# Kernel tuning notes

Hardware: AMD Instinct MI355X
Metric: run time of the kernel (lower is better)

Reference implementation:

```python
import jax, jax.numpy as jnp
import numpy as np

NUM_HEADS = 12
NUM_LANDMARKS = 64
DIM = 768


def _iterative_inv(mat, n_iter=6):
    # mat: [B, H, L, L]
    L = mat.shape[-1]
    I = jnp.eye(L, dtype=mat.dtype)
    K = mat
    # init: V = K^T / max_j(sum_i K_ij), scalar per (B, H)
    denom = jnp.max(jnp.sum(K, axis=-2), axis=-1)[:, :, None, None]
    V = (1.0 / denom) * jnp.swapaxes(K, -1, -2)
    for _ in range(n_iter):
        KV = jnp.matmul(K, V)
        V = jnp.matmul(0.25 * V, 13.0 * I - jnp.matmul(KV, 15.0 * I - jnp.matmul(KV, 7.0 * I - KV)))
    return V


def setup_inputs() -> dict:
    key = jax.random.key(0)
    k1, k2, k3, k4 = jax.random.split(key, 4)
    B, N, C = 4, 4096, DIM
    x = jax.random.normal(k1, (B, N, C), dtype=jnp.float32)
    w_qkv = jax.random.normal(k2, (3 * C, C), dtype=jnp.float32) * (C ** -0.5)
    w_proj = jax.random.normal(k3, (C, C), dtype=jnp.float32) * (C ** -0.5)
    b_proj = jax.random.normal(k4, (C,), dtype=jnp.float32) * 0.01
    return {"x": x, "w_qkv": w_qkv, "w_proj": w_proj, "b_proj": b_proj}


def reference(x, w_qkv, w_proj, b_proj):
    B, N, C = x.shape
    H, Lm = NUM_HEADS, NUM_LANDMARKS
    hd = C // H
    scale = hd ** 0.5
    # qkv: [3, B, H, N, hd]
    qkv = (x @ w_qkv.T).reshape(B, N, 3, H, hd).transpose(2, 0, 3, 1, 4)
    q, k, v = qkv[0], qkv[1], qkv[2]
    q = q / scale  # scaling happens BEFORE landmark pooling, as in source
    segs = N // Lm  # N % Lm == 0 path
    keys_landmarks = k.reshape(B, H, Lm, segs, hd).mean(axis=-2)      # [B,H,Lm,hd]
    queries_landmarks = q.reshape(B, H, Lm, segs, hd).mean(axis=-2)   # [B,H,Lm,hd]
    kernel_1 = jax.nn.softmax(jnp.einsum('bhnd,bhld->bhnl', q, keys_landmarks), axis=-1)            # [B,H,N,Lm]
    kernel_2 = jax.nn.softmax(jnp.einsum('bhmd,bhld->bhml', queries_landmarks, keys_landmarks), axis=-1)  # [B,H,Lm,Lm]
    kernel_3 = jax.nn.softmax(jnp.einsum('bhld,bhnd->bhln', queries_landmarks, k), axis=-1)         # [B,H,Lm,N]
    out = jnp.matmul(jnp.matmul(kernel_1, _iterative_inv(kernel_2)), jnp.matmul(kernel_3, v))       # [B,H,N,hd]
    out = out.transpose(0, 2, 1, 3).reshape(B, N, C)
    return out @ w_proj.T + b_proj
```

## Files before the change

kernel.cpp:

```cpp
#include <hip/hip_runtime.h>
#include <hip/hip_bf16.h>

#define DI __device__ __forceinline__

typedef __attribute__((ext_vector_type(8))) short bh8;
typedef __attribute__((ext_vector_type(8))) unsigned short us8;
typedef __attribute__((ext_vector_type(4))) float f4ev;

static constexpr int Bn = 4;
static constexpr int Nn = 4096;
static constexpr int Cn = 768;
static constexpr int Hn = 12;
static constexpr int Dn = 64;
static constexpr int Ln = 64;
static constexpr int TOKS = Bn * Nn;
static constexpr int BHn = Bn * Hn;

static constexpr size_t SZ_XB  = (size_t)TOKS * Cn * 2;
static constexpr size_t SZ_QKV = (size_t)BHn * Nn * Dn * 2;
static constexpr size_t OFF_XB   = 0;
static constexpr size_t OFF_QB   = OFF_XB + SZ_XB;
static constexpr size_t OFF_KB   = OFF_QB + SZ_QKV;
static constexpr size_t OFF_VB   = OFF_KB + SZ_QKV;
static constexpr size_t OFF_WQB  = OFF_VB + SZ_QKV;
static constexpr size_t OFF_WPB  = OFF_WQB + (size_t)3 * Cn * Cn * 2;
static constexpr size_t OFF_XM   = OFF_WPB + (size_t)Cn * Cn * 2;
static constexpr size_t OFF_QL   = OFF_XM + (size_t)Bn * Ln * Cn * 4;
static constexpr size_t OFF_KL   = OFF_QL + (size_t)Bn * Ln * Cn * 4;
static constexpr size_t OFF_VINV = OFF_KL + (size_t)Bn * Ln * Cn * 4;
static constexpr size_t OFF_CP   = OFF_VINV + (size_t)BHn * 64 * 64 * 4;
static constexpr size_t OFF_W2   = OFF_CP + (size_t)BHn * 32 * 64 * 2 * 4;

DI unsigned short f2bf(float f) {
  __hip_bfloat16 h = __float2bfloat16(f);
  return *reinterpret_cast<unsigned short*>(&h);
}
DI float bf2f(unsigned short u) {
  union { unsigned int i; float f; } c; c.i = ((unsigned)u) << 16; return c.f;
}

DI void gload_lds16(const void* g, void* l) {
  __builtin_amdgcn_global_load_lds((const __attribute__((address_space(1))) void*)g,
                                   (__attribute__((address_space(3))) void*)l, 16, 0, 0);
}

__global__ void castw_k(const float* __restrict__ wqkv, const float* __restrict__ wproj,
                        unsigned short* __restrict__ dq, unsigned short* __restrict__ dp) {
  const int nq = 3 * Cn * Cn / 4;
  const int np = Cn * Cn / 4;
  int i = blockIdx.x * blockDim.x + threadIdx.x;
  int st = gridDim.x * blockDim.x;
  for (; i < nq + np; i += st) {
    const float4* s4;
    ushort4* d4;
    int idx;
    if (i < nq) { s4 = (const float4*)wqkv;  d4 = (ushort4*)dq; idx = i; }
    else        { s4 = (const float4*)wproj; d4 = (ushort4*)dp; idx = i - nq; }
    float4 v = s4[idx];
    ushort4 o; o.x = f2bf(v.x); o.y = f2bf(v.y); o.z = f2bf(v.z); o.w = f2bf(v.w);
    d4[idx] = o;
  }
}

__global__ void castmean_k(const float* __restrict__ x, unsigned short* __restrict__ xb,
                           float* __restrict__ xm) {
  int bl = blockIdx.x, cz = blockIdx.y;
  int c = cz * 384 + threadIdx.x * 2;
  const float* xp = x + (size_t)bl * 64 * Cn + c;
  unsigned short* xbp = xb + (size_t)bl * 64 * Cn + c;
  float s0 = 0.f, s1 = 0.f;
  #pragma unroll 8
  for (int r = 0; r < 64; ++r) {
    float2 v = *(const float2*)(xp + (size_t)r * Cn);
    ushort2 o; o.x = f2bf(v.x); o.y = f2bf(v.y);
    *(ushort2*)(xbp + (size_t)r * Cn) = o;
    s0 += v.x; s1 += v.y;
  }
  xm[(size_t)bl * Cn + c]     = s0 * 0.015625f;
  xm[(size_t)bl * Cn + c + 1] = s1 * 0.015625f;
}

__launch_bounds__(256)
__global__ void landgemm_k(const float* __restrict__ xm, const float* __restrict__ wqkv,
                           float* __restrict__ part) {
  __shared__ float XT[64][65];
  __shared__ float WT[64][65];
  int b = blockIdx.x, ct = blockIdx.y, kc = blockIdx.z;
  int t = threadIdx.x;
  int tr = t >> 4, tc = t & 15;
  int r0 = tr * 4, j0 = tc * 4;
  const float* xb_ = xm + (size_t)b * Ln * Cn + kc * 64;
  const float* wb_ = wqkv + (size_t)ct * 64 * Cn + kc * 64;
  #pragma unroll
  for (int i = t; i < 1024; i += 256) {
    int r = i >> 4, c4 = (i & 15) * 4;
    float4 xv = *(const float4*)(xb_ + (size_t)r * Cn + c4);
    XT[c4 + 0][r] = xv.x; XT[c4 + 1][r] = xv.y; XT[c4 + 2][r] = xv.z; XT[c4 + 3][r] = xv.w;
    float4 wv = *(const float4*)(wb_ + (size_t)r * Cn + c4);
    WT[c4 + 0][r] = wv.x; WT[c4 + 1][r] = wv.y; WT[c4 + 2][r] = wv.z; WT[c4 + 3][r] = wv.w;
  }
  __syncthreads();
  float acc[4][4];
  #pragma unroll
  for (int i = 0; i < 4; ++i)
    #pragma unroll
    for (int j = 0; j < 4; ++j) acc[i][j] = 0.f;
  for (int cc = 0; cc < 64; ++cc) {
    float4 a4 = *(const float4*)&XT[cc][r0];
    float4 b4 = *(const float4*)&WT[cc][j0];
    acc[0][0] += a4.x * b4.x; acc[0][1] += a4.x * b4.y; acc[0][2] += a4.x * b4.z; acc[0][3] += a4.x * b4.w;
    acc[1][0] += a4.y * b4.x; acc[1][1] += a4.y * b4.y; acc[1][2] += a4.y * b4.z; acc[1][3] += a4.y * b4.w;
    acc[2][0] += a4.z * b4.x; acc[2][1] += a4.z * b4.y; acc[2][2] += a4.z * b4.z; acc[2][3] += a4.z * b4.w;
    acc[3][0] += a4.w * b4.x; acc[3][1] += a4.w * b4.y; acc[3][2] += a4.w * b4.z; acc[3][3] += a4.w * b4.w;
  }
  float* op = part + ((size_t)kc * 256 + b * Ln) * 1536 + (size_t)ct * 64;
  #pragma unroll
  for (int i = 0; i < 4; ++i)
    *(float4*)(op + (size_t)(r0 + i) * 1536 + j0) = make_float4(acc[i][0], acc[i][1], acc[i][2], acc[i][3]);
}

__global__ void landred_k(const float* __restrict__ part, float* __restrict__ ql,
                          float* __restrict__ kl) {
  int i4 = blockIdx.x * 256 + threadIdx.x;
  const float4* p4 = (const float4*)part;
  float4 s = p4[i4];
  #pragma unroll
  for (int kc = 1; kc < 12; ++kc) {
    float4 v = p4[(size_t)kc * 98304 + i4];
    s.x += v.x; s.y += v.y; s.z += v.z; s.w += v.w;
  }
  int row = i4 / 384, c = (i4 % 384) * 4;
  if (c < 768) {
    s.x *= 0.125f; s.y *= 0.125f; s.z *= 0.125f; s.w *= 0.125f;
    *(float4*)(ql + (size_t)row * Cn + c) = s;
  } else {
    *(float4*)(kl + (size_t)row * Cn + (c - 768)) = s;
  }
}

__launch_bounds__(256)
__global__ void k2inv_k(const float* __restrict__ ql, const float* __restrict__ kl,
                        float* __restrict__ vinv) {
  __shared__ float B0[64][68], B1[64][68], B2[64][68], B3[64][68],
                   B4[64][68], B5[64][68], B6[64][68], B7[64][68];
  __shared__ float dinv_s;
  float (*Qt)[68] = B0, (*Kt)[68] = B1;
  float (*KV)[68] = B0, (*KVt)[68] = B1;
  float (*K2)[68] = B2, (*K2t)[68] = B3;
  float (*Vv)[68] = B4, (*Vt)[68] = B5;
  float (*T1)[68] = B6, (*Uu)[68] = B7;

  int bh = blockIdx.x, b = bh / Hn, h = bh % Hn;
  int t = threadIdx.x;
  int tr = t >> 4, tc = t & 15;
  int r0 = tr * 4, j0 = tc * 4;

  {
    const float* qbase = ql + (size_t)(b * Ln) * Cn + h * Dn;
    const float* kbase = kl + (size_t)(b * Ln) * Cn + h * Dn;
    #pragma unroll
    for (int it = 0; it < 4; ++it) {
      int idx = it * 256 + t;
      int l = idx >> 4, d0 = (idx & 15) * 4;
      float4 qv = *(const float4*)(qbase + (size_t)l * Cn + d0);
      float4 kv = *(const float4*)(kbase + (size_t)l * Cn + d0);
      Qt[d0 + 0][l] = qv.x; Qt[d0 + 1][l] = qv.y; Qt[d0 + 2][l] = qv.z; Qt[d0 + 3][l] = qv.w;
      Kt[d0 + 0][l] = kv.x; Kt[d0 + 1][l] = kv.y; Kt[d0 + 2][l] = kv.z; Kt[d0 + 3][l] = kv.w;
    }
  }
  __syncthreads();

  float acc[4][4];
  #define MM64(LT, RR)                                                     \
    {                                                                      \
      _Pragma("unroll")                                                    \
      for (int i_ = 0; i_ < 4; ++i_)                                       \
        _Pragma("unroll")                                                  \
        for (int j_ = 0; j_ < 4; ++j_) acc[i_][j_] = 0.f;                  \
      for (int c_ = 0; c_ < 64; c_ += 4) {                                 \
        _Pragma("unroll")                                                  \
        for (int cc_ = 0; cc_ < 4; ++cc_) {                                \
          float4 a4 = *(const float4*)&LT[c_ + cc_][r0];                   \
          float4 b4 = *(const float4*)&RR[c_ + cc_][j0];                   \
          acc[0][0] += a4.x * b4.x; acc[0][1] += a4.x * b4.y;              \
          acc[0][2] += a4.x * b4.z; acc[0][3] += a4.x * b4.w;              \
          acc[1][0] += a4.y * b4.x; acc[1][1] += a4.y * b4.y;              \
          acc[1][2] += a4.y * b4.z; acc[1][3] += a4.y * b4.w;              \
          acc[2][0] += a4.z * b4.x; acc[2][1] += a4.z * b4.y;              \
          acc[2][2] += a4.z * b4.z; acc[2][3] += a4.z * b4.w;              \
          acc[3][0] += a4.w * b4.x; acc[3][1] += a4.w * b4.y;              \
          acc[3][2] += a4.w * b4.z; acc[3][3] += a4.w * b4.w;              \
        }                                                                  \
      }                                                                    \
    }

  MM64(Qt, Kt);
  #pragma unroll
  for (int i = 0; i < 4; ++i)
    *(float4*)&K2[r0 + i][j0] = make_float4(acc[i][0], acc[i][1], acc[i][2], acc[i][3]);
  __syncthreads();

  if (t < 64) {
    float m = -1e30f;
    #pragma unroll
    for (int c4 = 0; c4 < 16; ++c4) {
      float4 v = *(const float4*)&K2[t][c4 * 4];
      m = fmaxf(m, fmaxf(fmaxf(v.x, v.y), fmaxf(v.z, v.w)));
    }
    float s = 0.f;
    #pragma unroll
    for (int c4 = 0; c4 < 16; ++c4) {
      float4 v = *(const float4*)&K2[t][c4 * 4];
      v.x = __expf(v.x - m); v.y = __expf(v.y - m);
      v.z = __expf(v.z - m); v.w = __expf(v.w - m);
      s += v.x + v.y + v.z + v.w;
      *(float4*)&K2[t][c4 * 4] = v;
    }
    float inv = 1.f / s;
    #pragma unroll
    for (int c4 = 0; c4 < 16; ++c4) {
      float4 v = *(const float4*)&K2[t][c4 * 4];
      v.x *= inv; v.y *= inv; v.z *= inv; v.w *= inv;
      *(float4*)&K2[t][c4 * 4] = v;
      K2t[c4 * 4 + 0][t] = v.x; K2t[c4 * 4 + 1][t] = v.y;
      K2t[c4 * 4 + 2][t] = v.z; K2t[c4 * 4 + 3][t] = v.w;
    }
  }
  __syncthreads();
  if (t < 64) {
    float cs = 0.f;
    #pragma unroll
    for (int c4 = 0; c4 < 16; ++c4) {
      float4 v = *(const float4*)&K2t[t][c4 * 4];
      cs += v.x + v.y + v.z + v.w;
    }
    #pragma unroll
    for (int off = 1; off < 64; off <<= 1) cs = fmaxf(cs, __shfl_xor(cs, off));
    if (t == 0) dinv_s = 1.f / cs;
  }
  __syncthreads();
  float dinv = dinv_s;
  #pragma unroll
  for (int jj = 0; jj < 4; ++jj) {
    float4 k4 = *(const float4*)&K2[j0 + jj][r0];
    k4.x *= dinv; k4.y *= dinv; k4.z *= dinv; k4.w *= dinv;
    *(float4*)&Vt[j0 + jj][r0] = k4;
    Vv[r0 + 0][j0 + jj] = k4.x; Vv[r0 + 1][j0 + jj] = k4.y;
    Vv[r0 + 2][j0 + jj] = k4.z; Vv[r0 + 3][j0 + jj] = k4.w;
  }
  __syncthreads();

  float nv[4][4];
  for (int itn = 0; itn < 6; ++itn) {
    MM64(K2t, Vv);
    #pragma unroll
    for (int i = 0; i < 4; ++i)
      *(float4*)&KV[r0 + i][j0] = make_float4(acc[i][0], acc[i][1], acc[i][2], acc[i][3]);
    #pragma unroll
    for (int jj = 0; jj < 4; ++jj)
      *(float4*)&KVt[j0 + jj][r0] = make_float4(acc[0][jj], acc[1][jj], acc[2][jj], acc[3][jj]);
    __syncthreads();
    MM64(KVt, KV);
    #pragma unroll
    for (int i = 0; i < 4; ++i) {
      float4 kv4 = *(const float4*)&KV[r0 + i][j0];
      *(float4*)&T1[r0 + i][j0] = make_float4(7.f * kv4.x - acc[i][0], 7.f * kv4.y - acc[i][1],
                                              7.f * kv4.z - acc[i][2], 7.f * kv4.w - acc[i][3]);
    }
    __syncthreads();
    MM64(KVt, T1);
    #pragma unroll
    for (int i = 0; i < 4; ++i) {
      float4 kv4 = *(const float4*)&KV[r0 + i][j0];
      *(float4*)&Uu[r0 + i][j0] = make_float4(15.f * kv4.x - acc[i][0], 15.f * kv4.y - acc[i][1],
                                              15.f * kv4.z - acc[i][2], 15.f * kv4.w - acc[i][3]);
    }
    __syncthreads();
    MM64(Vt, Uu);
    #pragma unroll
    for (int i = 0; i < 4; ++i) {
      float4 v4 = *(const float4*)&Vv[r0 + i][j0];
      nv[i][0] = 0.25f * (13.f * v4.x - acc[i][0]);
      nv[i][1] = 0.25f * (13.f * v4.y - acc[i][1]);
      nv[i][2] = 0.25f * (13.f * v4.z - acc[i][2]);
      nv[i][3] = 0.25f * (13.f * v4.w - acc[i][3]);
    }
    __syncthreads();
    #pragma unroll
    for (int i = 0; i < 4; ++i)
      *(float4*)&Vv[r0 + i][j0] = make_float4(nv[i][0], nv[i][1], nv[i][2], nv[i][3]);
    #pragma unroll
    for (int jj = 0; jj < 4; ++jj)
      *(float4*)&Vt[j0 + jj][r0] = make_float4(nv[0][jj], nv[1][jj], nv[2][jj], nv[3][jj]);
    __syncthreads();
  }
  float* op = vinv + (size_t)bh * 4096;
  #pragma unroll
  for (int i = 0; i < 4; ++i)
    *(float4*)(op + (size_t)(r0 + i) * 64 + j0) = make_float4(nv[i][0], nv[i][1], nv[i][2], nv[i][3]);
  #undef MM64
}

__launch_bounds__(256)
__global__ void gemm_qkv_k(const __hip_bfloat16* __restrict__ A, const __hip_bfloat16* __restrict__ W,
                           __hip_bfloat16* __restrict__ qb, __hip_bfloat16* __restrict__ kb,
                           __hip_bfloat16* __restrict__ vb) {
  __shared__ unsigned short As[2][128][64], Bs[2][128][64];
  int t = threadIdx.x, lane = t & 63, w = t >> 6;
  int wr = w >> 1, wc = w & 1;
  int m0 = blockIdx.x * 128, n0 = blockIdx.y * 128;
  int srow = w * 8 + (lane >> 3);
  int scol = ((lane & 7) ^ ((lane >> 3) & 7)) * 8;
  f4ev acc[4][4];
  f4ev zz = {0.f, 0.f, 0.f, 0.f};
  #pragma unroll
  for (int m = 0; m < 4; ++m)
    #pragma unroll
    for (int n = 0; n < 4; ++n) acc[m][n] = zz;
  const __hip_bfloat16* ga = A + (size_t)(m0 + srow) * Cn + scol;
  const __hip_bfloat16* gb = W + (size_t)(n0 + srow) * Cn + scol;

  #pragma unroll
  for (int c = 0; c < 4; ++c) {
    gload_lds16(ga + (size_t)(c * 32) * Cn, &As[0][c * 32 + w * 8][0]);
    gload_lds16(gb + (size_t)(c * 32) * Cn, &Bs[0][c * 32 + w * 8][0]);
  }
  asm volatile("s_waitcnt vmcnt(0)" ::: "memory");
  __builtin_amdgcn_s_barrier();
  int cur = 0;
  for (int it = 0; it < 12; ++it) {
    if (it < 11) {
      int k0 = (it + 1) * 64;
      #pragma unroll
      for (int c = 0; c < 4; ++c) {
        gload_lds16(ga + (size_t)(c * 32) * Cn + k0, &As[cur ^ 1][c * 32 + w * 8][0]);
        gload_lds16(gb + (size_t)(c * 32) * Cn + k0, &Bs[cur ^ 1][c * 32 + w * 8][0]);
      }
      asm volatile("s_waitcnt vmcnt(8)" ::: "memory");
    } else {
      asm volatile("s_waitcnt vmcnt(0)" ::: "memory");
    }
    __builtin_amdgcn_s_barrier();
    #pragma unroll
    for (int ks = 0; ks < 2; ++ks) {
      int pc = ((ks * 4 + (lane >> 4)) ^ (lane & 7)) * 8;
      bh8 af[4], bf_[4];
      #pragma unroll
      for (int m = 0; m < 4; ++m)
        af[m] = *(const bh8*)&As[cur][wr * 64 + m * 16 + (lane & 15)][pc];
      #pragma unroll
      for (int n = 0; n < 4; ++n)
        bf_[n] = *(const bh8*)&Bs[cur][wc * 64 + n * 16 + (lane & 15)][pc];
      #pragma unroll
      for (int m = 0; m < 4; ++m)
        #pragma unroll
        for (int n = 0; n < 4; ++n)
          acc[m][n] = __builtin_amdgcn_mfma_f32_16x16x32_bf16(af[m], bf_[n], acc[m][n], 0, 0, 0);
    }
    asm volatile("s_waitcnt lgkmcnt(0)" ::: "memory");
    __builtin_amdgcn_s_barrier();
    cur ^= 1;
  }
  int which = (n0 >= 1536) ? 2 : (n0 >= 768 ? 1 : 0);
  __hip_bfloat16* dst = which == 0 ? qb : (which == 1 ? kb : vb);
  float sc = which == 0 ? 0.125f : 1.f;
  #pragma unroll
  for (int m = 0; m < 4; ++m) {
    int rbase = m0 + wr * 64 + m * 16 + ((lane >> 4) << 2);
    #pragma unroll
    for (int n = 0; n < 4; ++n) {
      int c = n0 + wc * 64 + n * 16 + (lane & 15);
      int rem = c - which * 768;
      int h = rem >> 6, dd = rem & 63;
      #pragma unroll
      for (int jj = 0; jj < 4; ++jj) {
        int r = rbase + jj;
        int b = r >> 12, ntok = r & 4095;
        dst[(((size_t)(b * Hn + h) * Nn + ntok) << 6) + dd] = __float2bfloat16(acc[m][n][jj] * sc);
      }
    }
  }
}

__launch_bounds__(256)
__global__ void k3vflash_k(const float* __restrict__ ql, const __hip_bfloat16* __restrict__ kb,
                           const __hip_bfloat16* __restrict__ vb,
                           float* __restrict__ ocp, float* __restrict__ stat) {
  __shared__ unsigned short Ks[128][72];
  __shared__ unsigned short VT[64][136];
  auto Pl = (unsigned short (*)[136]) & Ks[0][0];
  int ch = blockIdx.x, bh = blockIdx.y;
  int b = bh / Hn, h = bh % Hn;
  int t = threadIdx.x, lane = t & 63, w = t >> 6;

  {
    int row = t >> 1, half = (t & 1) * 32;
    const us8* krow = (const us8*)((const unsigned short*)kb + ((size_t)bh * Nn + (size_t)ch * 128 + row) * Dn + half);
    const us8* vrow = (const us8*)((const unsigned short*)vb + ((size_t)bh * Nn + (size_t)ch * 128 + row) * Dn + half);
    us8 kv0 = krow[0], kv1 = krow[1], kv2 = krow[2], kv3 = krow[3];
    us8 vv0 = vrow[0], vv1 = vrow[1], vv2 = vrow[2], vv3 = vrow[3];
    *(us8*)&Ks[row][half + 0]  = kv0;
    *(us8*)&Ks[row][half + 8]  = kv1;
    *(us8*)&Ks[row][half + 16] = kv2;
    *(us8*)&Ks[row][half + 24] = kv3;
    #pragma unroll
    for (int e = 0; e < 8; ++e) {
      VT[half + e][row]      = vv0[e];
      VT[half + 8 + e][row]  = vv1[e];
      VT[half + 16 + e][row] = vv2[e];
      VT[half + 24 + e][row] = vv3[e];
    }
  }
  bh8 aq[2];
  {
    const float* qrow = ql + ((size_t)(b * Ln + w * 16 + (lane & 15))) * Cn + h * Dn + (lane >> 4) * 8;
    #pragma unroll
    for (int ks = 0; ks < 2; ++ks) {
      float4 f0 = *(const float4*)(qrow + ks * 32);
      float4 f1 = *(const float4*)(qrow + ks * 32 + 4);
      bh8 v;
      v[0] = (short)f2bf(f0.x); v[1] = (short)f2bf(f0.y); v[2] = (short)f2bf(f0.z); v[3] = (short)f2bf(f0.w);
      v[4] = (short)f2bf(f1.x); v[5] = (short)f2bf(f1.y); v[6] = (short)f2bf(f1.z); v[7] = (short)f2bf(f1.w);
      aq[ks] = v;
    }
  }
  __syncthreads();
  f4ev sacc[8];
  f4ev zz = {0.f, 0.f, 0.f, 0.f};
  #pragma unroll
  for (int nt = 0; nt < 8; ++nt) sacc[nt] = zz;
  #pragma unroll
  for (int ks = 0; ks < 2; ++ks)
    #pragma unroll
    for (int nt = 0; nt < 8; ++nt) {
      bh8 bk = *(const bh8*)&Ks[nt * 16 + (lane & 15)][ks * 32 + (lane >> 4) * 8];
      sacc[nt] = __builtin_amdgcn_mfma_f32_16x16x32_bf16(aq[ks], bk, sacc[nt], 0, 0, 0);
    }
  float M[4];
  #pragma unroll
  for (int j = 0; j < 4; ++j) {
    float m = sacc[0][j];
    #pragma unroll
    for (int nt = 1; nt < 8; ++nt) m = fmaxf(m, sacc[nt][j]);
    m = fmaxf(m, __shfl_xor(m, 1));
    m = fmaxf(m, __shfl_xor(m, 2));
    m = fmaxf(m, __shfl_xor(m, 4));
    m = fmaxf(m, __shfl_xor(m, 8));
    M[j] = m;
  }
  __syncthreads();
  float Ssum[4] = {0.f, 0.f, 0.f, 0.f};
  #pragma unroll
  for (int nt = 0; nt < 8; ++nt)
    #pragma unroll
    for (int j = 0; j < 4; ++j) {
      float pf = __expf(sacc[nt][j] - M[j]);
      Ssum[j] += pf;
      Pl[w * 16 + (lane >> 4) * 4 + j][nt * 16 + (lane & 15)] = f2bf(pf);
    }
  #pragma unroll
  for (int j = 0; j < 4; ++j) {
    float s = Ssum[j];
    s += __shfl_xor(s, 1);
    s += __shfl_xor(s, 2);
    s += __shfl_xor(s, 4);
    s += __shfl_xor(s, 8);
    Ssum[j] = s;
  }
  if ((lane & 15) == 0) {
    #pragma unroll
    for (int j = 0; j < 4; ++j) {
      int l2 = w * 16 + (lane >> 4) * 4 + j;
      float* sp = stat + (((size_t)bh * 32 + ch) * 64 + l2) * 2;
      sp[0] = M[j]; sp[1] = Ssum[j];
    }
  }
  __syncthreads();
  f4ev oacc[4];
  #pragma unroll
  for (int nt = 0; nt < 4; ++nt) oacc[nt] = zz;
  #pragma unroll
  for (int ks = 0; ks < 4; ++ks) {
    bh8 ap = *(const bh8*)&Pl[w * 16 + (lane & 15)][ks * 32 + (lane >> 4) * 8];
    #pragma unroll
    for (int nt = 0; nt < 4; ++nt) {
      bh8 bv = *(const bh8*)&VT[nt * 16 + (lane & 15)][ks * 32 + (lane >> 4) * 8];
      oacc[nt] = __builtin_amdgcn_mfma_f32_16x16x32_bf16(ap, bv, oacc[nt], 0, 0, 0);
    }
  }
  float* ob = ocp + (((size_t)bh * 32 + ch) * 64) * 64;
  #pragma unroll
  for (int nt = 0; nt < 4; ++nt)
    #pragma unroll
    for (int j = 0; j < 4; ++j) {
      int l2 = w * 16 + ((lane >> 4) << 2) + j;
      ob[l2 * 64 + nt * 16 + (lane & 15)] = oacc[nt][j];
    }
}

__global__ void k3vcomb_k(float* __restrict__ ocp, const float* __restrict__ stat) {
  int bh = blockIdx.x, rg = blockIdx.y;
  int t = threadIdx.x;
  int row = rg * 4 + (t >> 6), col = t & 63;
  const float* sp = stat + (size_t)bh * 32 * 128 + row * 2;
  float M = -1e30f;
  #pragma unroll
  for (int c = 0; c < 32; ++c) M = fmaxf(M, sp[c * 128]);
  float S = 0.f;
  float wcb[32];
  #pragma unroll
  for (int c = 0; c < 32; ++c) {
    float wv = __expf(sp[c * 128] - M);
    wcb[c] = wv;
    S += wv * sp[c * 128 + 1];
  }
  float inv = 1.f / S;
  float* base = ocp + (size_t)bh * 32 * 4096 + row * 64 + col;
  float acc = 0.f;
  #pragma unroll
  for (int c = 0; c < 32; ++c) acc += base[(size_t)c * 4096] * wcb[c];
  *base = acc * inv;
}

__global__ void w2m_k(const float* __restrict__ ocp, const float* __restrict__ vinv,
                      float* __restrict__ w2) {
  __shared__ float kv[64][72], vi[64][72];
  int bh = blockIdx.x, t = threadIdx.x, j = t & 63, ig = t >> 6;
  for (int i = t; i < 4096; i += 256) {
    kv[i >> 6][i & 63] = ocp[(size_t)bh * 32 * 4096 + i];
    vi[i >> 6][i & 63] = vinv[(size_t)bh * 4096 + i];
  }
  __syncthreads();
  float a[16];
  #pragma unroll
  for (int li = 0; li < 16; ++li) a[li] = 0.f;
  for (int c2 = 0; c2 < 64; ++c2) {
    float vv = kv[c2][j];
    #pragma unroll
    for (int li = 0; li < 16; ++li) a[li] += vi[ig * 16 + li][c2] * vv;
  }
  #pragma unroll
  for (int li = 0; li < 16; ++li) w2[(size_t)bh * 4096 + (ig * 16 + li) * 64 + j] = a[li];
}

__launch_bounds__(256)
__global__ void k1app_k(const __hip_bfloat16* __restrict__ qb, const float* __restrict__ kl,
                        const float* __restrict__ w2, __hip_bfloat16* __restrict__ oh) {
  __shared__ unsigned short SM[128 * 72 + 64 * 72 * 2];
  auto Klhi = (unsigned short (*)[72])(SM);
  auto Kllo = (unsigned short (*)[72])(SM + 64 * 72);
  auto Pl   = (unsigned short (*)[72])(SM);
  auto Whi  = (unsigned short (*)[72])(SM + 128 * 72);
  auto Wlo  = (unsigned short (*)[72])(SM + 128 * 72 + 64 * 72);

  int ch = blockIdx.x, bh = blockIdx.y;
  int b = bh / Hn, h = bh % Hn;
  int t = threadIdx.x, lane = t & 63, w = t >> 6;

  {
    const float* klb = kl + (size_t)(b * Ln) * Cn + h * Dn;
    const float* w2b = w2 + (size_t)bh * 4096;
    #pragma unroll
    for (int it = 0; it < 4; ++it) {
      int idx = it * 256 + t;
      int l = idx >> 4, d0 = (idx & 15) * 4;
      float4 kv = *(const float4*)(klb + (size_t)l * Cn + d0);
      ushort4 hi4; ushort4 lo4;
      hi4.x = f2bf(kv.x); lo4.x = f2bf(kv.x - bf2f(hi4.x));
      hi4.y = f2bf(kv.y); lo4.y = f2bf(kv.y - bf2f(hi4.y));
      hi4.z = f2bf(kv.z); lo4.z = f2bf(kv.z - bf2f(hi4.z));
      hi4.w = f2bf(kv.w); lo4.w = f2bf(kv.w - bf2f(hi4.w));
      *(ushort4*)&Klhi[l][d0] = hi4;
      *(ushort4*)&Kllo[l][d0] = lo4;
      float4 wv = *(const float4*)(w2b + (size_t)l * 64 + d0);
      unsigned short h0 = f2bf(wv.x), h1 = f2bf(wv.y), h2 = f2bf(wv.z), h3 = f2bf(wv.w);
      Whi[d0 + 0][l] = h0; Wlo[d0 + 0][l] = f2bf(wv.x - bf2f(h0));
      Whi[d0 + 1][l] = h1; Wlo[d0 + 1][l] = f2bf(wv.y - bf2f(h1));
      Whi[d0 + 2][l] = h2; Wlo[d0 + 2][l] = f2bf(wv.z - bf2f(h2));
      Whi[d0 + 3][l] = h3; Wlo[d0 + 3][l] = f2bf(wv.w - bf2f(h3));
    }
  }
  bh8 aq[2][2];
  {
    const unsigned short* qbase = (const unsigned short*)qb + ((size_t)bh * Nn + (size_t)ch * 128) * Dn;
    #pragma unroll
    for (int m = 0; m < 2; ++m)
      #pragma unroll
      for (int ks = 0; ks < 2; ++ks)
        aq[m][ks] = *(const bh8*)(qbase + (size_t)(w * 32 + m * 16 + (lane & 15)) * Dn + ks * 32 + (lane >> 4) * 8);
  }
  __syncthreads();
  f4ev sacc[2][4];
  f4ev zz = {0.f, 0.f, 0.f, 0.f};
  #pragma unroll
  for (int m = 0; m < 2; ++m)
    #pragma unroll
    for (int nt = 0; nt < 4; ++nt) sacc[m][nt] = zz;
  #pragma unroll
  for (int ks = 0; ks < 2; ++ks)
    #pragma unroll
    for (int nt = 0; nt < 4; ++nt) {
      bh8 bhi = *(const bh8*)&Klhi[nt * 16 + (lane & 15)][ks * 32 + (lane >> 4) * 8];
      bh8 blo = *(const bh8*)&Kllo[nt * 16 + (lane & 15)][ks * 32 + (lane >> 4) * 8];
      #pragma unroll
      for (int m = 0; m < 2; ++m) {
        sacc[m][nt] = __builtin_amdgcn_mfma_f32_16x16x32_bf16(aq[m][ks], bhi, sacc[m][nt], 0, 0, 0);
        sacc[m][nt] = __builtin_amdgcn_mfma_f32_16x16x32_bf16(aq[m][ks], blo, sacc[m][nt], 0, 0, 0);
      }
    }
  float Pn[2][4][4];
  #pragma unroll
  for (int m = 0; m < 2; ++m)
    #pragma unroll
    for (int j = 0; j < 4; ++j) {
      float mx = sacc[m][0][j];
      #pragma unroll
      for (int nt = 1; nt < 4; ++nt) mx = fmaxf(mx, sacc[m][nt][j]);
      mx = fmaxf(mx, __shfl_xor(mx, 1));
      mx = fmaxf(mx, __shfl_xor(mx, 2));
      mx = fmaxf(mx, __shfl_xor(mx, 4));
      mx = fmaxf(mx, __shfl_xor(mx, 8));
      float sum = 0.f;
      #pragma unroll
      for (int nt = 0; nt < 4; ++nt) {
        float e = __expf(sacc[m][nt][j] - mx);
        Pn[m][nt][j] = e;
        sum += e;
      }
      sum += __shfl_xor(sum, 1);
      sum += __shfl_xor(sum, 2);
      sum += __shfl_xor(sum, 4);
      sum += __shfl_xor(sum, 8);
      float inv = 1.f / sum;
      #pragma unroll
      for (int nt = 0; nt < 4; ++nt) Pn[m][nt][j] *= inv;
    }
  __syncthreads();
  #pragma unroll
  for (int m = 0; m < 2; ++m)
    #pragma unroll
    for (int nt = 0; nt < 4; ++nt)
      #pragma unroll
      for (int j = 0; j < 4; ++j)
        Pl[w * 32 + m * 16 + (lane >> 4) * 4 + j][nt * 16 + (lane & 15)] = f2bf(Pn[m][nt][j]);
  __syncthreads();
  f4ev oacc[2][4];
  #pragma unroll
  for (int m = 0; m < 2; ++m)
    #pragma unroll
    for (int nt = 0; nt < 4; ++nt) oacc[m][nt] = zz;
  #pragma unroll
  for (int ks = 0; ks < 2; ++ks) {
    bh8 ap[2];
    #pragma unroll
    for (int m = 0; m < 2; ++m)
      ap[m] = *(const bh8*)&Pl[w * 32 + m * 16 + (lane & 15)][ks * 32 + (lane >> 4) * 8];
    #pragma unroll
    for (int nt = 0; nt < 4; ++nt) {
      bh8 bhi = *(const bh8*)&Whi[nt * 16 + (lane & 15)][ks * 32 + (lane >> 4) * 8];
      bh8 blo = *(const bh8*)&Wlo[nt * 16 + (lane & 15)][ks * 32 + (lane >> 4) * 8];
      #pragma unroll
      for (int m = 0; m < 2; ++m) {
        oacc[m][nt] = __builtin_amdgcn_mfma_f32_16x16x32_bf16(ap[m], bhi, oacc[m][nt], 0, 0, 0);
        oacc[m][nt] = __builtin_amdgcn_mfma_f32_16x16x32_bf16(ap[m], blo, oacc[m][nt], 0, 0, 0);
      }
    }
  }
  unsigned short* ohb = (unsigned short*)oh;
  #pragma unroll
  for (int m = 0; m < 2; ++m)
    #pragma unroll
    for (int nt = 0; nt < 4; ++nt)
      #pragma unroll
      for (int j = 0; j < 4; ++j) {
        int tok = ch * 128 + w * 32 + m * 16 + (lane >> 4) * 4 + j;
        int dd = nt * 16 + (lane & 15);
        ohb[((size_t)(b * Nn + tok)) * Cn + h * Dn + dd] = f2bf(oacc[m][nt][j]);
      }
}

__launch_bounds__(256)
__global__ void gemm_proj_k(const __hip_bfloat16* __restrict__ A, const __hip_bfloat16* __restrict__ W,
                            const float* __restrict__ bias, float* __restrict__ out) {
  __shared__ unsigned short As[128][32], Bs[128][32];
  int t = threadIdx.x, lane = t & 63, w = t >> 6;
  int wr = w >> 1, wc = w & 1;
  int m0 = blockIdx.x * 128, n0 = blockIdx.y * 128;
  int srow = lane >> 2;
  int scol = (((lane & 3) ^ ((lane >> 3) & 3))) * 8;
  int rcol = (((lane >> 4) ^ ((lane >> 1) & 3))) * 8;
  f4ev acc[4][4];
  f4ev zz = {0.f, 0.f, 0.f, 0.f};
  #pragma unroll
  for (int m = 0; m < 4; ++m)
    #pragma unroll
    for (int n = 0; n < 4; ++n) acc[m][n] = zz;
  const __hip_bfloat16* ga = A + (size_t)(m0 + w * 16 + srow) * Cn + scol;
  const __hip_bfloat16* gb = W + (size_t)(n0 + w * 16 + srow) * Cn + scol;
  for (int k0 = 0; k0 < Cn; k0 += 32) {
    gload_lds16(ga + k0,                   &As[w * 16][0]);
    gload_lds16(ga + (size_t)64 * Cn + k0, &As[64 + w * 16][0]);
    gload_lds16(gb + k0,                   &Bs[w * 16][0]);
    gload_lds16(gb + (size_t)64 * Cn + k0, &Bs[64 + w * 16][0]);
    __syncthreads();
    bh8 af[4], bf_[4];
    #pragma unroll
    for (int m = 0; m < 4; ++m)
      af[m] = *(const bh8*)&As[wr * 64 + m * 16 + (lane & 15)][rcol];
    #pragma unroll
    for (int n = 0; n < 4; ++n)
      bf_[n] = *(const bh8*)&Bs[wc * 64 + n * 16 + (lane & 15)][rcol];
    #pragma unroll
    for (int m = 0; m < 4; ++m)
      #pragma unroll
      for (int n = 0; n < 4; ++n)
        acc[m][n] = __builtin_amdgcn_mfma_f32_16x16x32_bf16(af[m], bf_[n], acc[m][n], 0, 0, 0);
    __syncthreads();
  }
  #pragma unroll
  for (int m = 0; m < 4; ++m) {
    int rbase = m0 + wr * 64 + m * 16 + ((lane >> 4) << 2);
    #pragma unroll
    for (int n = 0; n < 4; ++n) {
      int c = n0 + wc * 64 + n * 16 + (lane & 15);
      float bv = bias[c];
      #pragma unroll
      for (int jj = 0; jj < 4; ++jj)
        out[(size_t)(rbase + jj) * Cn + c] = acc[m][n][jj] + bv;
    }
  }
}

extern "C" void kernel_launch(void* const* d_in, const int* in_sizes, int n_in,
                              void* d_out, int out_size, void* d_ws, size_t ws_size,
                              hipStream_t stream) {
  const float* x     = (const float*)d_in[0];
  const float* wqkv  = (const float*)d_in[1];
  const float* wproj = (const float*)d_in[2];
  const float* bproj = (const float*)d_in[3];
  float* out = (float*)d_out;
  char* ws = (char*)d_ws;

  auto xb   = (__hip_bfloat16*)(ws + OFF_XB);
  auto qb   = (__hip_bfloat16*)(ws + OFF_QB);
  auto kb   = (__hip_bfloat16*)(ws + OFF_KB);
  auto vb   = (__hip_bfloat16*)(ws + OFF_VB);
  auto wqb  = (__hip_bfloat16*)(ws + OFF_WQB);
  auto wpb  = (__hip_bfloat16*)(ws + OFF_WPB);
  auto ocp  = (float*)(ws + OFF_XB);
  auto oh   = (__hip_bfloat16*)(ws + OFF_XB);
  auto part = (float*)(ws + OFF_QB);
  auto xm   = (float*)(ws + OFF_XM);
  auto ql   = (float*)(ws + OFF_QL);
  auto kl   = (float*)(ws + OFF_KL);
  auto vinv = (float*)(ws + OFF_VINV);
  auto cp   = (float*)(ws + OFF_CP);
  auto w2   = (float*)(ws + OFF_W2);

  castmean_k<<<dim3(256, 2), 192, 0, stream>>>(x, (unsigned short*)xb, xm);
  castw_k<<<1536, 256, 0, stream>>>(wqkv, wproj, (unsigned short*)wqb, (unsigned short*)wpb);
  landgemm_k<<<dim3(4, 24, 12), 256, 0, stream>>>(xm, wqkv, part);
  landred_k<<<384, 256, 0, stream>>>(part, ql, kl);
  k2inv_k<<<48, 256, 0, stream>>>(ql, kl, vinv);
  gemm_qkv_k<<<dim3(128, 18), 256, 0, stream>>>(xb, wqb, qb, kb, vb);
  k3vflash_k<<<dim3(32, 48), 256, 0, stream>>>(ql, kb, vb, ocp, cp);
  k3vcomb_k<<<dim3(48, 16), 256, 0, stream>>>(ocp, cp);
  w2m_k<<<48, 256, 0, stream>>>(ocp, vinv, w2);
  k1app_k<<<dim3(32, 48), 256, 0, stream>>>(qb, kl, w2, oh);
  gemm_proj_k<<<dim3(128, 6), 256, 0, stream>>>(oh, wpb, bproj, out);
}
```

Before: 255.6 us.

## Double-buffer projection GEMM LDS tiles and widen the K step

```diff
diff --git a/kernel.cpp b/kernel.cpp
--- a/kernel.cpp
+++ b/kernel.cpp
@@ -682,40 +682,61 @@
 __launch_bounds__(256)
 __global__ void gemm_proj_k(const __hip_bfloat16* __restrict__ A, const __hip_bfloat16* __restrict__ W,
                             const float* __restrict__ bias, float* __restrict__ out) {
-  __shared__ unsigned short As[128][32], Bs[128][32];
+  __shared__ unsigned short As[2][128][64], Bs[2][128][64];
   int t = threadIdx.x, lane = t & 63, w = t >> 6;
   int wr = w >> 1, wc = w & 1;
   int m0 = blockIdx.x * 128, n0 = blockIdx.y * 128;
-  int srow = lane >> 2;
-  int scol = (((lane & 3) ^ ((lane >> 3) & 3))) * 8;
-  int rcol = (((lane >> 4) ^ ((lane >> 1) & 3))) * 8;
+  int srow = w * 8 + (lane >> 3);
+  int scol = ((lane & 7) ^ ((lane >> 3) & 7)) * 8;
   f4ev acc[4][4];
   f4ev zz = {0.f, 0.f, 0.f, 0.f};
   #pragma unroll
   for (int m = 0; m < 4; ++m)
     #pragma unroll
     for (int n = 0; n < 4; ++n) acc[m][n] = zz;
-  const __hip_bfloat16* ga = A + (size_t)(m0 + w * 16 + srow) * Cn + scol;
-  const __hip_bfloat16* gb = W + (size_t)(n0 + w * 16 + srow) * Cn + scol;
-  for (int k0 = 0; k0 < Cn; k0 += 32) {
-    gload_lds16(ga + k0,                   &As[w * 16][0]);
-    gload_lds16(ga + (size_t)64 * Cn + k0, &As[64 + w * 16][0]);
-    gload_lds16(gb + k0,                   &Bs[w * 16][0]);
-    gload_lds16(gb + (size_t)64 * Cn + k0, &Bs[64 + w * 16][0]);
-    __syncthreads();
-    bh8 af[4], bf_[4];
-    #pragma unroll
-    for (int m = 0; m < 4; ++m)
-      af[m] = *(const bh8*)&As[wr * 64 + m * 16 + (lane & 15)][rcol];
-    #pragma unroll
-    for (int n = 0; n < 4; ++n)
-      bf_[n] = *(const bh8*)&Bs[wc * 64 + n * 16 + (lane & 15)][rcol];
-    #pragma unroll
-    for (int m = 0; m < 4; ++m)
+  const __hip_bfloat16* ga = A + (size_t)(m0 + srow) * Cn + scol;
+  const __hip_bfloat16* gb = W + (size_t)(n0 + srow) * Cn + scol;
+
+  #pragma unroll
+  for (int c = 0; c < 4; ++c) {
+    gload_lds16(ga + (size_t)(c * 32) * Cn, &As[0][c * 32 + w * 8][0]);
+    gload_lds16(gb + (size_t)(c * 32) * Cn, &Bs[0][c * 32 + w * 8][0]);
+  }
+  asm volatile("s_waitcnt vmcnt(0)" ::: "memory");
+  __builtin_amdgcn_s_barrier();
+  int cur = 0;
+  for (int it = 0; it < 12; ++it) {
+    if (it < 11) {
+      int k0 = (it + 1) * 64;
+      #pragma unroll
+      for (int c = 0; c < 4; ++c) {
+        gload_lds16(ga + (size_t)(c * 32) * Cn + k0, &As[cur ^ 1][c * 32 + w * 8][0]);
+        gload_lds16(gb + (size_t)(c * 32) * Cn + k0, &Bs[cur ^ 1][c * 32 + w * 8][0]);
+      }
+      asm volatile("s_waitcnt vmcnt(8)" ::: "memory");
+    } else {
+      asm volatile("s_waitcnt vmcnt(0)" ::: "memory");
+    }
+    __builtin_amdgcn_s_barrier();
+    #pragma unroll
+    for (int ks = 0; ks < 2; ++ks) {
+      int pc = ((ks * 4 + (lane >> 4)) ^ (lane & 7)) * 8;
+      bh8 af[4], bf_[4];
+      #pragma unroll
+      for (int m = 0; m < 4; ++m)
+        af[m] = *(const bh8*)&As[cur][wr * 64 + m * 16 + (lane & 15)][pc];
       #pragma unroll
       for (int n = 0; n < 4; ++n)
-        acc[m][n] = __builtin_amdgcn_mfma_f32_16x16x32_bf16(af[m], bf_[n], acc[m][n], 0, 0, 0);
-    __syncthreads();
+        bf_[n] = *(const bh8*)&Bs[cur][wc * 64 + n * 16 + (lane & 15)][pc];
+      #pragma unroll
+      for (int m = 0; m < 4; ++m)
+        #pragma unroll
+        for (int n = 0; n < 4; ++n)
+          acc[m][n] = __builtin_amdgcn_mfma_f32_16x16x32_bf16(af[m], bf_[n], acc[m][n], 0, 0, 0);
+    }
+    asm volatile("s_waitcnt lgkmcnt(0)" ::: "memory");
+    __builtin_amdgcn_s_barrier();
+    cur ^= 1;
   }
   #pragma unroll
   for (int m = 0; m < 4; ++m) {
```

Result: slower. 266.8 us (+4.4%).
